# Performance work log

Hardware: AMD Instinct MI355X
Metric: run time of the kernel (lower is better)

The kernel has to match this reference:

```python
import jax, jax.numpy as jnp
import numpy as np

B, T, D_IN, H, D_OUT = 256, 512, 64, 256, 8


def setup_inputs() -> dict:
    key = jax.random.key(0)
    ks = jax.random.split(key, 6)
    s_ih = 1.0 / np.sqrt(H)
    inputs = jax.random.normal(ks[0], (B, T, D_IN), dtype=jnp.float32)
    h0 = jnp.zeros((B, H), dtype=jnp.float32)
    c0 = jnp.zeros((B, H), dtype=jnp.float32)
    # LSTM cell params, PyTorch gate order (i, f, g, o)
    W_ih = jax.random.uniform(ks[1], (4 * H, D_IN), minval=-s_ih, maxval=s_ih, dtype=jnp.float32)
    W_hh = jax.random.uniform(ks[2], (4 * H, H), minval=-s_ih, maxval=s_ih, dtype=jnp.float32)
    b = jax.random.uniform(ks[3], (4 * H,), minval=-s_ih, maxval=s_ih, dtype=jnp.float32)
    # output projection (xavier_uniform weight, zero bias)
    lim = np.sqrt(6.0 / (H + D_OUT))
    W_out = jax.random.uniform(ks[4], (D_OUT, H), minval=-lim, maxval=lim, dtype=jnp.float32)
    b_out = jnp.zeros((D_OUT,), dtype=jnp.float32)
    return {"inputs": inputs, "h0": h0, "c0": c0, "W_ih": W_ih, "W_hh": W_hh,
            "b": b, "W_out": W_out, "b_out": b_out}


def _lstm_last(inputs, h0, c0, W_ih, W_hh, b):
    # inputs: [B, T, D_in] -> scan over time, keep only final hidden state
    xs = jnp.swapaxes(inputs, 0, 1)  # [T, B, D_in]

    def step(carry, x_t):
        h, c = carry
        gates = x_t @ W_ih.T + h @ W_hh.T + b  # [B, 4H]
        i, f, g, o = jnp.split(gates, 4, axis=-1)
        c_new = jax.nn.sigmoid(f) * c + jax.nn.sigmoid(i) * jnp.tanh(g)
        h_new = jax.nn.sigmoid(o) * jnp.tanh(c_new)
        return (h_new, c_new), None

    (h, c), _ = jax.lax.scan(step, (h0, c0), xs)
    return h, c


def reference(inputs, h0, c0, W_ih, W_hh, b, W_out, b_out):
    h, c = _lstm_last(inputs, h0, c0, W_ih, W_hh, b)
    rnn_outputs = h  # last-timestep output (dropout_prob=0 -> identity)
    logits = rnn_outputs @ W_out.T + b_out
    return (rnn_outputs, logits, h, c)
```

## Files before the change

kernel.cpp:

```cpp
#include <hip/hip_runtime.h>

#define T_ 512
#define B_ 256
#define H_ 256
#define DIN_ 64

typedef __attribute__((ext_vector_type(8))) short short8;
typedef __attribute__((ext_vector_type(4))) float f32x4;
typedef __attribute__((ext_vector_type(4))) unsigned int u32x4;

__device__ __forceinline__ unsigned short f2bf(float f) {
  unsigned u = __float_as_uint(f);
  u += 0x7FFFu + ((u >> 16) & 1u);
  return (unsigned short)(u >> 16);
}
__device__ __forceinline__ float bf2f(unsigned short s) {
  return __uint_as_float(((unsigned)s) << 16);
}
__device__ __forceinline__ float sigm(float x) { return 1.0f / (1.0f + __expf(-x)); }
__device__ __forceinline__ float tanh_(float x) {
  float xx = fminf(fmaxf(x, -30.0f), 30.0f);
  float e = __expf(2.0f * xx);
  return (e - 1.0f) / (e + 1.0f);
}

__device__ __forceinline__ void load16_sc1(const unsigned* p, u32x4& a,
                                           u32x4& b, u32x4& c, u32x4& d) {
  asm volatile(
      "global_load_dwordx4 %0, %4, off sc1\n\t"
      "global_load_dwordx4 %1, %4, off offset:16 sc1\n\t"
      "global_load_dwordx4 %2, %4, off offset:32 sc1\n\t"
      "global_load_dwordx4 %3, %4, off offset:48 sc1\n\t"
      "s_waitcnt vmcnt(0)"
      : "=v"(a), "=v"(b), "=v"(c), "=v"(d)
      : "v"(p) : "memory");
}

__device__ __forceinline__ bool tags_ok(u32x4 a, u32x4 b, u32x4 c, u32x4 d,
                                        unsigned w) {
  unsigned m = (a.x >> 16) ^ w; m |= (a.y >> 16) ^ w;
  m |= (a.z >> 16) ^ w;         m |= (a.w >> 16) ^ w;
  m |= (b.x >> 16) ^ w;         m |= (b.y >> 16) ^ w;
  m |= (b.z >> 16) ^ w;         m |= (b.w >> 16) ^ w;
  m |= (c.x >> 16) ^ w;         m |= (c.y >> 16) ^ w;
  m |= (c.z >> 16) ^ w;         m |= (c.w >> 16) ^ w;
  m |= (d.x >> 16) ^ w;         m |= (d.y >> 16) ^ w;
  m |= (d.z >> 16) ^ w;         m |= (d.w >> 16) ^ w;
  return m == 0;
}

__global__ __launch_bounds__(256) void lstm_kern(
    const float* __restrict__ xin, const float* __restrict__ h0f,
    const float* __restrict__ c0f, const float* __restrict__ Wih,
    const float* __restrict__ Whh, const float* __restrict__ bias,
    const float* __restrict__ Wout, const float* __restrict__ bout,
    float* __restrict__ out, unsigned* hbuf32)
{
  const int tid = threadIdx.x;
  const int gb  = blockIdx.x >> 4;
  const int gc  = blockIdx.x & 15;
  const int wv  = tid >> 6;
  const int ln  = tid & 63;
  const int colB = ln & 15;
  const int krow = ln >> 4;

  __shared__ unsigned short h_s[16 * 264];
  __shared__ unsigned short x_s[16 * 72];
  __shared__ float gbuf[4 * 16 * 17];

  const int j = wv * H_ + gc * 16 + colB;
  short8 bh[8], bx[2];
  #pragma unroll
  for (int kc = 0; kc < 8; ++kc) {
    const float* p = Whh + j * H_ + kc * 32 + krow * 8;
    short8 f;
    #pragma unroll
    for (int i = 0; i < 8; ++i) f[i] = (short)f2bf(p[i]);
    bh[kc] = f;
  }
  #pragma unroll
  for (int kc = 0; kc < 2; ++kc) {
    const float* p = Wih + j * DIN_ + kc * 32 + krow * 8;
    short8 f;
    #pragma unroll
    for (int i = 0; i < 8; ++i) f[i] = (short)f2bf(p[i]);
    bx[kc] = f;
  }
  const float bval = bias[j];

  const int er = tid >> 4, ec = tid & 15;
  const int grow = gb * 16 + er;
  float c_val = c0f[grow * H_ + gc * 16 + ec];
  float h_val = 0.0f;

  const int hr = tid >> 4;
  const int hcb = (tid & 15) * 16;
  const unsigned* ldp_base = hbuf32 + gb * 4096 + hr * 256 + hcb;
  unsigned* stp_base = hbuf32 + gb * 4096 + er * 256 + gc * 16 + ec;

  for (int s = 1; s <= T_; ++s) {
    {
      int r = tid >> 4, d4 = (tid & 15) * 4;
      float4 v = *(const float4*)(xin + ((gb * 16 + r) * T_ + (s - 1)) * DIN_ + d4);
      unsigned short* q = &x_s[r * 72 + d4];
      q[0] = f2bf(v.x); q[1] = f2bf(v.y); q[2] = f2bf(v.z); q[3] = f2bf(v.w);
    }

    if (s == 1) {
      #pragma unroll
      for (int it = 0; it < 4; ++it) {
        int e4 = tid + it * 256;
        int r = e4 >> 6, c4 = e4 & 63;
        const float4* p = (const float4*)(h0f + (gb * 16 + r) * H_) + c4;
        float4 v = *p;
        unsigned short* q = &h_s[r * 264 + c4 * 4];
        q[0] = f2bf(v.x); q[1] = f2bf(v.y); q[2] = f2bf(v.z); q[3] = f2bf(v.w);
      }
    } else {
      const unsigned want = (unsigned)(s - 1);
      const unsigned* ldp = ldp_base + (((s - 1) & 1) << 16);
      u32x4 va, vb, vc, vd;
      int tries = 0;
      do {
        load16_sc1(ldp, va, vb, vc, vd);
        if (tags_ok(va, vb, vc, vd, want)) break;
      } while (++tries < (1 << 18));
      unsigned* q32 = (unsigned*)&h_s[hr * 264 + hcb];
      q32[0] = (va.x & 0xFFFFu) | (va.y << 16);
      q32[1] = (va.z & 0xFFFFu) | (va.w << 16);
      q32[2] = (vb.x & 0xFFFFu) | (vb.y << 16);
      q32[3] = (vb.z & 0xFFFFu) | (vb.w << 16);
      q32[4] = (vc.x & 0xFFFFu) | (vc.y << 16);
      q32[5] = (vc.z & 0xFFFFu) | (vc.w << 16);
      q32[6] = (vd.x & 0xFFFFu) | (vd.y << 16);
      q32[7] = (vd.z & 0xFFFFu) | (vd.w << 16);
    }
    __syncthreads();

    f32x4 acc = {0.f, 0.f, 0.f, 0.f};
    #pragma unroll
    for (int kc = 0; kc < 2; ++kc) {
      short8 a = *(const short8*)&x_s[colB * 72 + kc * 32 + krow * 8];
      acc = __builtin_amdgcn_mfma_f32_16x16x32_bf16(a, bx[kc], acc, 0, 0, 0);
    }
    #pragma unroll
    for (int kc = 0; kc < 8; ++kc) {
      short8 a = *(const short8*)&h_s[colB * 264 + kc * 32 + krow * 8];
      acc = __builtin_amdgcn_mfma_f32_16x16x32_bf16(a, bh[kc], acc, 0, 0, 0);
    }
    #pragma unroll
    for (int i = 0; i < 4; ++i)
      gbuf[wv * 272 + (krow * 4 + i) * 17 + colB] = acc[i] + bval;
    __syncthreads();

    float gi = gbuf[0 * 272 + er * 17 + ec];
    float gf = gbuf[1 * 272 + er * 17 + ec];
    float gg = gbuf[2 * 272 + er * 17 + ec];
    float go = gbuf[3 * 272 + er * 17 + ec];
    c_val = sigm(gf) * c_val + sigm(gi) * tanh_(gg);
    h_val = sigm(go) * tanh_(c_val);

    unsigned pk = ((unsigned)s << 16) | (unsigned)f2bf(h_val);
    __hip_atomic_store(stp_base + ((s & 1) << 16), pk,
                       __ATOMIC_RELAXED, __HIP_MEMORY_SCOPE_AGENT);
  }

  const int gj = gc * 16 + ec;
  out[grow * H_ + gj] = h_val;
  out[67584 + grow * H_ + gj] = h_val;
  out[133120 + grow * H_ + gj] = c_val;

  if (gc == 0) {
    const unsigned want = (unsigned)T_;
    const unsigned* ldp = ldp_base + ((T_ & 1) << 16);
    u32x4 va, vb, vc, vd;
    int tries = 0;
    do {
      load16_sc1(ldp, va, vb, vc, vd);
      if (tags_ok(va, vb, vc, vd, want)) break;
    } while (++tries < (1 << 18));
    unsigned* q32 = (unsigned*)&h_s[hr * 264 + hcb];
    q32[0] = (va.x & 0xFFFFu) | (va.y << 16);
    q32[1] = (va.z & 0xFFFFu) | (va.w << 16);
    q32[2] = (vb.x & 0xFFFFu) | (vb.y << 16);
    q32[3] = (vb.z & 0xFFFFu) | (vb.w << 16);
    q32[4] = (vc.x & 0xFFFFu) | (vc.y << 16);
    q32[5] = (vc.z & 0xFFFFu) | (vc.w << 16);
    q32[6] = (vd.x & 0xFFFFu) | (vd.y << 16);
    q32[7] = (vd.z & 0xFFFFu) | (vd.w << 16);
    __syncthreads();
    if (tid < 128) {
      int r = tid >> 3, o = tid & 7;
      float a = bout[o];
      for (int k = 0; k < H_; ++k)
        a = fmaf(bf2f(h_s[r * 264 + k]), Wout[o * H_ + k], a);
      out[65536 + (gb * 16 + r) * 8 + o] = a;
    }
  }
}

extern "C" void kernel_launch(void* const* d_in, const int* in_sizes, int n_in,
                              void* d_out, int out_size, void* d_ws, size_t ws_size,
                              hipStream_t stream) {
  const float* xin  = (const float*)d_in[0];
  const float* h0f  = (const float*)d_in[1];
  const float* c0f  = (const float*)d_in[2];
  const float* Wih  = (const float*)d_in[3];
  const float* Whh  = (const float*)d_in[4];
  const float* bias = (const float*)d_in[5];
  const float* Wout = (const float*)d_in[6];
  const float* bout = (const float*)d_in[7];
  float* out = (float*)d_out;

  unsigned* hbuf32 = (unsigned*)d_ws;

  void* args[] = {&xin, &h0f, &c0f, &Wih, &Whh, &bias, &Wout, &bout,
                  &out, &hbuf32};
  hipLaunchCooperativeKernel((void*)lstm_kern, dim3(256), dim3(256),
                             args, 0, stream);
}
```

Baseline: 1.173 ms.

## Process two batch groups per block, interleaving their recurrent steps to hide sync latency

Each block now owns two 16-row batch groups and alternates their LSTM steps, so waiting on one group's cross-block hidden-state exchange can overlap with compute on the other. The grid is halved to 128 blocks. The next timestep's input x is also prefetched into registers one step ahead. The cost is double the serial work per block per step and more LDS, while the per-step critical path through the spin-wait still remains.

```diff
diff --git a/kernel.cpp b/kernel.cpp
--- a/kernel.cpp
+++ b/kernel.cpp
@@ -57,75 +57,86 @@
     float* __restrict__ out, unsigned* hbuf32)
 {
   const int tid = threadIdx.x;
-  const int gb  = blockIdx.x >> 4;
+  const int p   = blockIdx.x >> 4;
   const int gc  = blockIdx.x & 15;
+  const int gbA = p * 2;
+  const int gbB = p * 2 + 1;
   const int wv  = tid >> 6;
   const int ln  = tid & 63;
   const int colB = ln & 15;
   const int krow = ln >> 4;
 
-  __shared__ unsigned short h_s[16 * 264];
-  __shared__ unsigned short x_s[16 * 72];
-  __shared__ float gbuf[4 * 16 * 17];
+  __shared__ unsigned short h_sA[16 * 264], h_sB[16 * 264];
+  __shared__ unsigned short x_sA[16 * 72],  x_sB[16 * 72];
+  __shared__ float gbufA[4 * 16 * 17], gbufB[4 * 16 * 17];
 
   const int j = wv * H_ + gc * 16 + colB;
   short8 bh[8], bx[2];
   #pragma unroll
   for (int kc = 0; kc < 8; ++kc) {
-    const float* p = Whh + j * H_ + kc * 32 + krow * 8;
+    const float* q = Whh + j * H_ + kc * 32 + krow * 8;
     short8 f;
     #pragma unroll
-    for (int i = 0; i < 8; ++i) f[i] = (short)f2bf(p[i]);
+    for (int i = 0; i < 8; ++i) f[i] = (short)f2bf(q[i]);
     bh[kc] = f;
   }
   #pragma unroll
   for (int kc = 0; kc < 2; ++kc) {
-    const float* p = Wih + j * DIN_ + kc * 32 + krow * 8;
+    const float* q = Wih + j * DIN_ + kc * 32 + krow * 8;
     short8 f;
     #pragma unroll
-    for (int i = 0; i < 8; ++i) f[i] = (short)f2bf(p[i]);
+    for (int i = 0; i < 8; ++i) f[i] = (short)f2bf(q[i]);
     bx[kc] = f;
   }
   const float bval = bias[j];
 
   const int er = tid >> 4, ec = tid & 15;
-  const int grow = gb * 16 + er;
-  float c_val = c0f[grow * H_ + gc * 16 + ec];
-  float h_val = 0.0f;
+  const int gj = gc * 16 + ec;
+  float c_valA = c0f[(gbA * 16 + er) * H_ + gj];
+  float c_valB = c0f[(gbB * 16 + er) * H_ + gj];
+  float h_valA = 0.0f, h_valB = 0.0f;
+
+  const int xr = tid >> 4, xd = (tid & 15) * 4;
+  const float* xrowA = xin + (gbA * 16 + xr) * (T_ * DIN_) + xd;
+  const float* xrowB = xin + (gbB * 16 + xr) * (T_ * DIN_) + xd;
+  float4 xcurA = *(const float4*)(xrowA);
+  float4 xcurB = *(const float4*)(xrowB);
 
   const int hr = tid >> 4;
   const int hcb = (tid & 15) * 16;
-  const unsigned* ldp_base = hbuf32 + gb * 4096 + hr * 256 + hcb;
-  unsigned* stp_base = hbuf32 + gb * 4096 + er * 256 + gc * 16 + ec;
+  const unsigned* ldpA_base = hbuf32 + gbA * 4096 + hr * 256 + hcb;
+  const unsigned* ldpB_base = hbuf32 + gbB * 4096 + hr * 256 + hcb;
+  unsigned* stpA = hbuf32 + gbA * 4096 + er * 256 + gj;
+  unsigned* stpB = hbuf32 + gbB * 4096 + er * 256 + gj;
 
   for (int s = 1; s <= T_; ++s) {
-    {
-      int r = tid >> 4, d4 = (tid & 15) * 4;
-      float4 v = *(const float4*)(xin + ((gb * 16 + r) * T_ + (s - 1)) * DIN_ + d4);
-      unsigned short* q = &x_s[r * 72 + d4];
-      q[0] = f2bf(v.x); q[1] = f2bf(v.y); q[2] = f2bf(v.z); q[3] = f2bf(v.w);
-    }
-
+    const int tn = (s < T_) ? s : (T_ - 1);
+
+    {
+      unsigned short* q = &x_sA[xr * 72 + xd];
+      q[0] = f2bf(xcurA.x); q[1] = f2bf(xcurA.y);
+      q[2] = f2bf(xcurA.z); q[3] = f2bf(xcurA.w);
+      xcurA = *(const float4*)(xrowA + tn * DIN_);
+    }
     if (s == 1) {
       #pragma unroll
       for (int it = 0; it < 4; ++it) {
         int e4 = tid + it * 256;
         int r = e4 >> 6, c4 = e4 & 63;
-        const float4* p = (const float4*)(h0f + (gb * 16 + r) * H_) + c4;
-        float4 v = *p;
-        unsigned short* q = &h_s[r * 264 + c4 * 4];
+        float4 v = ((const float4*)(h0f + (gbA * 16 + r) * H_))[c4];
+        unsigned short* q = &h_sA[r * 264 + c4 * 4];
         q[0] = f2bf(v.x); q[1] = f2bf(v.y); q[2] = f2bf(v.z); q[3] = f2bf(v.w);
       }
     } else {
       const unsigned want = (unsigned)(s - 1);
-      const unsigned* ldp = ldp_base + (((s - 1) & 1) << 16);
+      const unsigned* ldp = ldpA_base + (((s - 1) & 1) << 16);
       u32x4 va, vb, vc, vd;
       int tries = 0;
       do {
         load16_sc1(ldp, va, vb, vc, vd);
         if (tags_ok(va, vb, vc, vd, want)) break;
       } while (++tries < (1 << 18));
-      unsigned* q32 = (unsigned*)&h_s[hr * 264 + hcb];
+      unsigned* q32 = (unsigned*)&h_sA[hr * 264 + hcb];
       q32[0] = (va.x & 0xFFFFu) | (va.y << 16);
       q32[1] = (va.z & 0xFFFFu) | (va.w << 16);
       q32[2] = (vb.x & 0xFFFFu) | (vb.y << 16);
@@ -137,64 +148,162 @@
     }
     __syncthreads();
 
-    f32x4 acc = {0.f, 0.f, 0.f, 0.f};
-    #pragma unroll
-    for (int kc = 0; kc < 2; ++kc) {
-      short8 a = *(const short8*)&x_s[colB * 72 + kc * 32 + krow * 8];
-      acc = __builtin_amdgcn_mfma_f32_16x16x32_bf16(a, bx[kc], acc, 0, 0, 0);
-    }
-    #pragma unroll
-    for (int kc = 0; kc < 8; ++kc) {
-      short8 a = *(const short8*)&h_s[colB * 264 + kc * 32 + krow * 8];
-      acc = __builtin_amdgcn_mfma_f32_16x16x32_bf16(a, bh[kc], acc, 0, 0, 0);
-    }
-    #pragma unroll
-    for (int i = 0; i < 4; ++i)
-      gbuf[wv * 272 + (krow * 4 + i) * 17 + colB] = acc[i] + bval;
-    __syncthreads();
-
-    float gi = gbuf[0 * 272 + er * 17 + ec];
-    float gf = gbuf[1 * 272 + er * 17 + ec];
-    float gg = gbuf[2 * 272 + er * 17 + ec];
-    float go = gbuf[3 * 272 + er * 17 + ec];
-    c_val = sigm(gf) * c_val + sigm(gi) * tanh_(gg);
-    h_val = sigm(go) * tanh_(c_val);
-
-    unsigned pk = ((unsigned)s << 16) | (unsigned)f2bf(h_val);
-    __hip_atomic_store(stp_base + ((s & 1) << 16), pk,
-                       __ATOMIC_RELAXED, __HIP_MEMORY_SCOPE_AGENT);
-  }
-
-  const int gj = gc * 16 + ec;
-  out[grow * H_ + gj] = h_val;
-  out[67584 + grow * H_ + gj] = h_val;
-  out[133120 + grow * H_ + gj] = c_val;
+    {
+      f32x4 acc = {0.f, 0.f, 0.f, 0.f};
+      #pragma unroll
+      for (int kc = 0; kc < 2; ++kc) {
+        short8 a = *(const short8*)&x_sA[colB * 72 + kc * 32 + krow * 8];
+        acc = __builtin_amdgcn_mfma_f32_16x16x32_bf16(a, bx[kc], acc, 0, 0, 0);
+      }
+      #pragma unroll
+      for (int kc = 0; kc < 8; ++kc) {
+        short8 a = *(const short8*)&h_sA[colB * 264 + kc * 32 + krow * 8];
+        acc = __builtin_amdgcn_mfma_f32_16x16x32_bf16(a, bh[kc], acc, 0, 0, 0);
+      }
+      #pragma unroll
+      for (int i = 0; i < 4; ++i)
+        gbufA[wv * 272 + (krow * 4 + i) * 17 + colB] = acc[i] + bval;
+    }
+    __syncthreads();
+
+    {
+      float gi = gbufA[0 * 272 + er * 17 + ec];
+      float gf = gbufA[1 * 272 + er * 17 + ec];
+      float gg = gbufA[2 * 272 + er * 17 + ec];
+      float go = gbufA[3 * 272 + er * 17 + ec];
+      c_valA = sigm(gf) * c_valA + sigm(gi) * tanh_(gg);
+      h_valA = sigm(go) * tanh_(c_valA);
+      unsigned pk = ((unsigned)s << 16) | (unsigned)f2bf(h_valA);
+      __hip_atomic_store(stpA + ((s & 1) << 16), pk,
+                         __ATOMIC_RELAXED, __HIP_MEMORY_SCOPE_AGENT);
+    }
+
+    {
+      unsigned short* q = &x_sB[xr * 72 + xd];
+      q[0] = f2bf(xcurB.x); q[1] = f2bf(xcurB.y);
+      q[2] = f2bf(xcurB.z); q[3] = f2bf(xcurB.w);
+      xcurB = *(const float4*)(xrowB + tn * DIN_);
+    }
+    if (s == 1) {
+      #pragma unroll
+      for (int it = 0; it < 4; ++it) {
+        int e4 = tid + it * 256;
+        int r = e4 >> 6, c4 = e4 & 63;
+        float4 v = ((const float4*)(h0f + (gbB * 16 + r) * H_))[c4];
+        unsigned short* q = &h_sB[r * 264 + c4 * 4];
+        q[0] = f2bf(v.x); q[1] = f2bf(v.y); q[2] = f2bf(v.z); q[3] = f2bf(v.w);
+      }
+    } else {
+      const unsigned want = (unsigned)(s - 1);
+      const unsigned* ldp = ldpB_base + (((s - 1) & 1) << 16);
+      u32x4 va, vb, vc, vd;
+      int tries = 0;
+      do {
+        load16_sc1(ldp, va, vb, vc, vd);
+        if (tags_ok(va, vb, vc, vd, want)) break;
+      } while (++tries < (1 << 18));
+      unsigned* q32 = (unsigned*)&h_sB[hr * 264 + hcb];
+      q32[0] = (va.x & 0xFFFFu) | (va.y << 16);
+      q32[1] = (va.z & 0xFFFFu) | (va.w << 16);
+      q32[2] = (vb.x & 0xFFFFu) | (vb.y << 16);
+      q32[3] = (vb.z & 0xFFFFu) | (vb.w << 16);
+      q32[4] = (vc.x & 0xFFFFu) | (vc.y << 16);
+      q32[5] = (vc.z & 0xFFFFu) | (vc.w << 16);
+      q32[6] = (vd.x & 0xFFFFu) | (vd.y << 16);
+      q32[7] = (vd.z & 0xFFFFu) | (vd.w << 16);
+    }
+    __syncthreads();
+
+    {
+      f32x4 acc = {0.f, 0.f, 0.f, 0.f};
+      #pragma unroll
+      for (int kc = 0; kc < 2; ++kc) {
+        short8 a = *(const short8*)&x_sB[colB * 72 + kc * 32 + krow * 8];
+        acc = __builtin_amdgcn_mfma_f32_16x16x32_bf16(a, bx[kc], acc, 0, 0, 0);
+      }
+      #pragma unroll
+      for (int kc = 0; kc < 8; ++kc) {
+        short8 a = *(const short8*)&h_sB[colB * 264 + kc * 32 + krow * 8];
+        acc = __builtin_amdgcn_mfma_f32_16x16x32_bf16(a, bh[kc], acc, 0, 0, 0);
+      }
+      #pragma unroll
+      for (int i = 0; i < 4; ++i)
+        gbufB[wv * 272 + (krow * 4 + i) * 17 + colB] = acc[i] + bval;
+    }
+    __syncthreads();
+
+    {
+      float gi = gbufB[0 * 272 + er * 17 + ec];
+      float gf = gbufB[1 * 272 + er * 17 + ec];
+      float gg = gbufB[2 * 272 + er * 17 + ec];
+      float go = gbufB[3 * 272 + er * 17 + ec];
+      c_valB = sigm(gf) * c_valB + sigm(gi) * tanh_(gg);
+      h_valB = sigm(go) * tanh_(c_valB);
+      unsigned pk = ((unsigned)s << 16) | (unsigned)f2bf(h_valB);
+      __hip_atomic_store(stpB + ((s & 1) << 16), pk,
+                         __ATOMIC_RELAXED, __HIP_MEMORY_SCOPE_AGENT);
+    }
+  }
+
+  {
+    const int growA = gbA * 16 + er;
+    const int growB = gbB * 16 + er;
+    out[growA * H_ + gj] = h_valA;
+    out[67584 + growA * H_ + gj] = h_valA;
+    out[133120 + growA * H_ + gj] = c_valA;
+    out[growB * H_ + gj] = h_valB;
+    out[67584 + growB * H_ + gj] = h_valB;
+    out[133120 + growB * H_ + gj] = c_valB;
+  }
 
   if (gc == 0) {
     const unsigned want = (unsigned)T_;
-    const unsigned* ldp = ldp_base + ((T_ & 1) << 16);
-    u32x4 va, vb, vc, vd;
-    int tries = 0;
-    do {
-      load16_sc1(ldp, va, vb, vc, vd);
-      if (tags_ok(va, vb, vc, vd, want)) break;
-    } while (++tries < (1 << 18));
-    unsigned* q32 = (unsigned*)&h_s[hr * 264 + hcb];
-    q32[0] = (va.x & 0xFFFFu) | (va.y << 16);
-    q32[1] = (va.z & 0xFFFFu) | (va.w << 16);
-    q32[2] = (vb.x & 0xFFFFu) | (vb.y << 16);
-    q32[3] = (vb.z & 0xFFFFu) | (vb.w << 16);
-    q32[4] = (vc.x & 0xFFFFu) | (vc.y << 16);
-    q32[5] = (vc.z & 0xFFFFu) | (vc.w << 16);
-    q32[6] = (vd.x & 0xFFFFu) | (vd.y << 16);
-    q32[7] = (vd.z & 0xFFFFu) | (vd.w << 16);
+    {
+      const unsigned* ldp = ldpA_base + ((T_ & 1) << 16);
+      u32x4 va, vb, vc, vd;
+      int tries = 0;
+      do {
+        load16_sc1(ldp, va, vb, vc, vd);
+        if (tags_ok(va, vb, vc, vd, want)) break;
+      } while (++tries < (1 << 18));
+      unsigned* q32 = (unsigned*)&h_sA[hr * 264 + hcb];
+      q32[0] = (va.x & 0xFFFFu) | (va.y << 16);
+      q32[1] = (va.z & 0xFFFFu) | (va.w << 16);
+      q32[2] = (vb.x & 0xFFFFu) | (vb.y << 16);
+      q32[3] = (vb.z & 0xFFFFu) | (vb.w << 16);
+      q32[4] = (vc.x & 0xFFFFu) | (vc.y << 16);
+      q32[5] = (vc.z & 0xFFFFu) | (vc.w << 16);
+      q32[6] = (vd.x & 0xFFFFu) | (vd.y << 16);
+      q32[7] = (vd.z & 0xFFFFu) | (vd.w << 16);
+    }
+    {
+      const unsigned* ldp = ldpB_base + ((T_ & 1) << 16);
+      u32x4 va, vb, vc, vd;
+      int tries = 0;
+      do {
+        load16_sc1(ldp, va, vb, vc, vd);
+        if (tags_ok(va, vb, vc, vd, want)) break;
+      } while (++tries < (1 << 18));
+      unsigned* q32 = (unsigned*)&h_sB[hr * 264 + hcb];
+      q32[0] = (va.x & 0xFFFFu) | (va.y << 16);
+      q32[1] = (va.z & 0xFFFFu) | (va.w << 16);
+      q32[2] = (vb.x & 0xFFFFu) | (vb.y << 16);
+      q32[3] = (vb.z & 0xFFFFu) | (vb.w << 16);
+      q32[4] = (vc.x & 0xFFFFu) | (vc.y << 16);
+      q32[5] = (vc.z & 0xFFFFu) | (vc.w << 16);
+      q32[6] = (vd.x & 0xFFFFu) | (vd.y << 16);
+      q32[7] = (vd.z & 0xFFFFu) | (vd.w << 16);
+    }
     __syncthreads();
     if (tid < 128) {
       int r = tid >> 3, o = tid & 7;
-      float a = bout[o];
-      for (int k = 0; k < H_; ++k)
-        a = fmaf(bf2f(h_s[r * 264 + k]), Wout[o * H_ + k], a);
-      out[65536 + (gb * 16 + r) * 8 + o] = a;
+      float aA = bout[o], aB = bout[o];
+      for (int k = 0; k < H_; ++k) {
+        aA = fmaf(bf2f(h_sA[r * 264 + k]), Wout[o * H_ + k], aA);
+        aB = fmaf(bf2f(h_sB[r * 264 + k]), Wout[o * H_ + k], aB);
+      }
+      out[65536 + (gbA * 16 + r) * 8 + o] = aA;
+      out[65536 + (gbB * 16 + r) * 8 + o] = aB;
     }
   }
 }
@@ -216,6 +325,6 @@
 
   void* args[] = {&xin, &h0f, &c0f, &Wih, &Whh, &bias, &Wout, &bout,
                   &out, &hbuf32};
-  hipLaunchCooperativeKernel((void*)lstm_kern, dim3(256), dim3(256),
+  hipLaunchCooperativeKernel((void*)lstm_kern, dim3(128), dim3(256),
                              args, 0, stream);
 }
```

Measured after the change: 1.802 ms. 53.7% more time.
